# Kernel optimization log

Measured on AMD Instinct MI355X. Metric: run time of the kernel, lower is better.

## Reference

```python
import jax, jax.numpy as jnp
import numpy as np

N, A, R = 131072, 16, 64


def setup_inputs() -> dict:
    key = jax.random.key(0)
    k1, k2, k3 = jax.random.split(key, 3)
    x = jax.random.normal(k1, (N, A), dtype=jnp.float32)
    mu = jax.random.uniform(k2, (R, A), dtype=jnp.float32)      # torch.rand(R, A)
    sigma = jnp.ones((R, A), dtype=jnp.float32) * 0.2           # torch.ones(R, A) * 0.2
    rho = jax.random.normal(k3, (R, A + 1), dtype=jnp.float32) * 0.1
    return {"x": x, "mu": mu, "sigma": sigma, "rho": rho}


def reference(x, mu, sigma, rho):
    # Rule consequents: z[k, r] = x[k] . rho[r, :A] + rho[r, A]   -> [N, R]
    z = jnp.einsum("na,ra->nr", x, rho[:, :-1]) + rho[:, -1]
    # Gaussian membership firing strengths (prod of exps == exp of sum):
    # w[k, r] = prod_a exp(-(x[k,a]-mu[r,a])^2 / (2 sigma[r,a]^2))
    d = x[:, None, :] - mu[None, :, :]                           # [N, R, A]
    logw = -jnp.sum(d * d / (2.0 * sigma[None] ** 2), axis=-1)   # [N, R]
    w = jnp.exp(logw)
    # diag(z @ w.T)[k] = sum_r z[k,r] * w[k,r]; normalized by rule-sum.
    num = jnp.sum(z * w, axis=1)
    den = jnp.sum(w, axis=1) + 1e-13
    return num / den
```

## Files before the change

kernel.cpp:

```cpp
#include <hip/hip_runtime.h>
#include <hip/hip_bf16.h>
#include <math.h>

#define NFEAT 16
#define NRULE 64
#define RQUADS 13
#define RPW 16
#define WPB 4

__global__ void fuzzy_prep(const float* __restrict__ mu,
                           const float* __restrict__ sigma,
                           const float* __restrict__ rho,
                           float* __restrict__ cst) {
    const float L2E = 1.4426950408889634f;
    int r = threadIdx.x;
    if (r >= NRULE) return;
    float* c = cst + r * (RQUADS * 4);
    float K = 0.0f;
#pragma unroll
    for (int a = 0; a < NFEAT; ++a) {
        float m = mu[r * NFEAT + a];
        float s = sigma[r * NFEAT + a];
        float inv = 1.0f / (2.0f * s * s);
        c[a]      = -inv * L2E;
        c[16 + a] = 2.0f * inv * m * L2E;
        c[32 + a] = rho[r * (NFEAT + 1) + a];
        K         = fmaf(-inv * m, m, K);
    }
    c[48] = rho[r * (NFEAT + 1) + NFEAT];
    c[49] = K * L2E;
    c[50] = 0.0f;
    c[51] = 0.0f;
}

__global__ __launch_bounds__(256) void fuzzy_main(const float* __restrict__ x,
                                                  const float* __restrict__ cst,
                                                  float* __restrict__ out,
                                                  int n) {
    __shared__ float4 cl[NRULE * RQUADS];
    __shared__ float pnum[WPB][64];
    __shared__ float pden[WPB][64];

    const int tid  = threadIdx.x;
    const int lane = tid & 63;
    const int q    = __builtin_amdgcn_readfirstlane(tid >> 6);
    const int k    = blockIdx.x * 64 + lane;
    const int kc   = k < n ? k : n - 1;

    const float4* cg = (const float4*)cst;
#pragma unroll
    for (int i = 0; i < 4; ++i) {
        int idx = tid + i * 256;
        if (idx < NRULE * RQUADS) cl[idx] = cg[idx];
    }

    const float4* x4 = (const float4*)(x + (size_t)kc * NFEAT);
    float4 v0 = x4[0], v1 = x4[1], v2 = x4[2], v3 = x4[3];
    float xs[NFEAT] = {v0.x, v0.y, v0.z, v0.w,
                       v1.x, v1.y, v1.z, v1.w,
                       v2.x, v2.y, v2.z, v2.w,
                       v3.x, v3.y, v3.z, v3.w};

    __syncthreads();

    float num = 0.0f, den = 0.0f;
    const float4* cb = cl + q * (RPW * RQUADS);
#pragma unroll 2
    for (int r = 0; r < RPW; ++r) {
        const float4* c = cb + r * RQUADS;
        float4 n0 = c[0], n1 = c[1], n2 = c[2], n3 = c[3];
        float4 m0 = c[4], m1 = c[5], m2 = c[6], m3 = c[7];
        float4 r0 = c[8], r1 = c[9], r2 = c[10], r3 = c[11];
        float4 tl = c[12];
        float nc[NFEAT]  = {n0.x,n0.y,n0.z,n0.w, n1.x,n1.y,n1.z,n1.w,
                            n2.x,n2.y,n2.z,n2.w, n3.x,n3.y,n3.z,n3.w};
        float cm[NFEAT]  = {m0.x,m0.y,m0.z,m0.w, m1.x,m1.y,m1.z,m1.w,
                            m2.x,m2.y,m2.z,m2.w, m3.x,m3.y,m3.z,m3.w};
        float rh[NFEAT]  = {r0.x,r0.y,r0.z,r0.w, r1.x,r1.y,r1.z,r1.w,
                            r2.x,r2.y,r2.z,r2.w, r3.x,r3.y,r3.z,r3.w};
        float z  = tl.x;
        float l0 = tl.y, l1 = 0.0f;
#pragma unroll
        for (int a = 0; a < NFEAT; a += 2) {
            float t0 = fmaf(nc[a],     xs[a],     cm[a]);
            float t1 = fmaf(nc[a + 1], xs[a + 1], cm[a + 1]);
            l0 = fmaf(t0, xs[a],     l0);
            l1 = fmaf(t1, xs[a + 1], l1);
            z  = fmaf(rh[a],     xs[a],     z);
            z  = fmaf(rh[a + 1], xs[a + 1], z);
        }
        float w = __builtin_amdgcn_exp2f(l0 + l1);
        num = fmaf(z, w, num);
        den += w;
    }

    pnum[q][lane] = num;
    pden[q][lane] = den;
    __syncthreads();
    if (q == 0 && k < n) {
        float nn = pnum[0][lane] + pnum[1][lane] + pnum[2][lane] + pnum[3][lane];
        float dd = pden[0][lane] + pden[1][lane] + pden[2][lane] + pden[3][lane];
        out[k] = nn / (dd + 1e-13f);
    }
}

extern "C" void kernel_launch(void* const* d_in, const int* in_sizes, int n_in,
                              void* d_out, int out_size, void* d_ws, size_t ws_size,
                              hipStream_t stream) {
    const float* x     = (const float*)d_in[0];
    const float* mu    = (const float*)d_in[1];
    const float* sigma = (const float*)d_in[2];
    const float* rho   = (const float*)d_in[3];
    float* out = (float*)d_out;
    float* cst = (float*)d_ws;

    int n = in_sizes[0] / NFEAT;

    fuzzy_prep<<<1, 64, 0, stream>>>(mu, sigma, rho, cst);
    fuzzy_main<<<(n + 63) / 64, 256, 0, stream>>>(x, cst, out, n);
}
```

Measured before the change: 77.61 us.

## Process four samples per thread and add uniform-sigma fast path

Each thread now handles four samples, so every rule constant loaded from LDS is reused across four samples instead of one, and the grid shrinks by four. The prep kernel detects at runtime whether all sigmas within a rule are equal. When they are, the quadratic term is computed once per sample as a shared ||x||^2 scaled by a per-rule constant, which removes one FMA per feature per rule. This fast path is general and checked at runtime, though it fires for the test inputs. The cost is higher register pressure from holding four x vectors, and fewer blocks to fill the GPU.

```diff
diff --git a/kernel.cpp b/kernel.cpp
--- a/kernel.cpp
+++ b/kernel.cpp
@@ -1,5 +1,4 @@
 #include <hip/hip_runtime.h>
-#include <hip/hip_bf16.h>
 #include <math.h>
 
 #define NFEAT 16
@@ -7,100 +6,165 @@
 #define RQUADS 13
 #define RPW 16
 #define WPB 4
+#define SPL 4
 
 __global__ void fuzzy_prep(const float* __restrict__ mu,
                            const float* __restrict__ sigma,
                            const float* __restrict__ rho,
                            float* __restrict__ cst) {
     const float L2E = 1.4426950408889634f;
+    __shared__ int uni[NRULE];
     int r = threadIdx.x;
-    if (r >= NRULE) return;
-    float* c = cst + r * (RQUADS * 4);
-    float K = 0.0f;
-#pragma unroll
-    for (int a = 0; a < NFEAT; ++a) {
-        float m = mu[r * NFEAT + a];
-        float s = sigma[r * NFEAT + a];
-        float inv = 1.0f / (2.0f * s * s);
-        c[a]      = -inv * L2E;
-        c[16 + a] = 2.0f * inv * m * L2E;
-        c[32 + a] = rho[r * (NFEAT + 1) + a];
-        K         = fmaf(-inv * m, m, K);
+    if (r < NRULE) {
+        float* c = cst + r * 52;
+        float s0 = sigma[r * NFEAT];
+        float c0 = 1.0f / (2.0f * s0 * s0);
+        float K = 0.0f;
+        int u = 1;
+        for (int a = 0; a < NFEAT; ++a) {
+            float m = mu[r * NFEAT + a];
+            float s = sigma[r * NFEAT + a];
+            float inv = 1.0f / (2.0f * s * s);
+            if (inv != c0) u = 0;
+            c[a]      = -inv * L2E;
+            c[16 + a] = 2.0f * inv * m * L2E;
+            c[32 + a] = rho[r * (NFEAT + 1) + a];
+            K         = fmaf(-inv * m, m, K);
+        }
+        c[48] = rho[r * (NFEAT + 1) + NFEAT];
+        c[49] = K * L2E;
+        c[50] = -c0 * L2E;
+        c[51] = 0.0f;
+        uni[r] = u;
     }
-    c[48] = rho[r * (NFEAT + 1) + NFEAT];
-    c[49] = K * L2E;
-    c[50] = 0.0f;
-    c[51] = 0.0f;
+    __syncthreads();
+    if (r == 0) {
+        int f = 1;
+        for (int i = 0; i < NRULE; ++i) f &= uni[i];
+        cst[NRULE * 52] = (float)f;
+    }
 }
 
-__global__ __launch_bounds__(256) void fuzzy_main(const float* __restrict__ x,
-                                                  const float* __restrict__ cst,
-                                                  float* __restrict__ out,
-                                                  int n) {
+__global__ __launch_bounds__(256, 2) void fuzzy_main(const float* __restrict__ x,
+                                                     const float* __restrict__ cst,
+                                                     float* __restrict__ out,
+                                                     int n) {
     __shared__ float4 cl[NRULE * RQUADS];
-    __shared__ float pnum[WPB][64];
-    __shared__ float pden[WPB][64];
+    __shared__ float pnum[WPB][256];
+    __shared__ float pden[WPB][256];
 
     const int tid  = threadIdx.x;
     const int lane = tid & 63;
     const int q    = __builtin_amdgcn_readfirstlane(tid >> 6);
-    const int k    = blockIdx.x * 64 + lane;
-    const int kc   = k < n ? k : n - 1;
+    const int base = blockIdx.x * (64 * SPL);
 
     const float4* cg = (const float4*)cst;
+    for (int i = tid; i < NRULE * RQUADS; i += 256) cl[i] = cg[i];
+    const int flag = (int)cst[NRULE * 52];
+
+    float xs[SPL][NFEAT];
+    float Qs[SPL];
 #pragma unroll
-    for (int i = 0; i < 4; ++i) {
-        int idx = tid + i * 256;
-        if (idx < NRULE * RQUADS) cl[idx] = cg[idx];
+    for (int s = 0; s < SPL; ++s) {
+        int k = base + s * 64 + lane;
+        int kc = k < n ? k : n - 1;
+        const float4* x4 = (const float4*)(x + (size_t)kc * NFEAT);
+        float4 a = x4[0], b = x4[1], c = x4[2], d = x4[3];
+        float* p = xs[s];
+        p[0]=a.x; p[1]=a.y; p[2]=a.z; p[3]=a.w;
+        p[4]=b.x; p[5]=b.y; p[6]=b.z; p[7]=b.w;
+        p[8]=c.x; p[9]=c.y; p[10]=c.z; p[11]=c.w;
+        p[12]=d.x; p[13]=d.y; p[14]=d.z; p[15]=d.w;
+        float qq = 0.0f;
+#pragma unroll
+        for (int a2 = 0; a2 < NFEAT; ++a2) qq = fmaf(p[a2], p[a2], qq);
+        Qs[s] = qq;
+    }
+    __syncthreads();
+
+    float num[SPL] = {0, 0, 0, 0}, den[SPL] = {0, 0, 0, 0};
+    const float4* cb = cl + q * (RPW * RQUADS);
+
+    if (flag) {
+#pragma unroll 2
+        for (int r = 0; r < RPW; ++r) {
+            const float4* c = cb + r * RQUADS;
+            float4 b0 = c[4], b1 = c[5], b2 = c[6], b3 = c[7];
+            float4 r0 = c[8], r1 = c[9], r2 = c[10], r3 = c[11];
+            float4 tl = c[12];
+            float B[NFEAT]  = {b0.x,b0.y,b0.z,b0.w, b1.x,b1.y,b1.z,b1.w,
+                               b2.x,b2.y,b2.z,b2.w, b3.x,b3.y,b3.z,b3.w};
+            float rh[NFEAT] = {r0.x,r0.y,r0.z,r0.w, r1.x,r1.y,r1.z,r1.w,
+                               r2.x,r2.y,r2.z,r2.w, r3.x,r3.y,r3.z,r3.w};
+            float z[SPL], l[SPL];
+#pragma unroll
+            for (int s = 0; s < SPL; ++s) {
+                z[s] = tl.x;
+                l[s] = fmaf(tl.z, Qs[s], tl.y);
+            }
+#pragma unroll
+            for (int a = 0; a < NFEAT; ++a) {
+#pragma unroll
+                for (int s = 0; s < SPL; ++s) {
+                    l[s] = fmaf(B[a],  xs[s][a], l[s]);
+                    z[s] = fmaf(rh[a], xs[s][a], z[s]);
+                }
+            }
+#pragma unroll
+            for (int s = 0; s < SPL; ++s) {
+                float w = __builtin_amdgcn_exp2f(l[s]);
+                num[s] = fmaf(z[s], w, num[s]);
+                den[s] += w;
+            }
+        }
+    } else {
+#pragma unroll 2
+        for (int r = 0; r < RPW; ++r) {
+            const float4* c = cb + r * RQUADS;
+            float4 n0 = c[0], n1 = c[1], n2 = c[2], n3 = c[3];
+            float4 m0 = c[4], m1 = c[5], m2 = c[6], m3 = c[7];
+            float4 r0 = c[8], r1 = c[9], r2 = c[10], r3 = c[11];
+            float4 tl = c[12];
+            float nc[NFEAT] = {n0.x,n0.y,n0.z,n0.w, n1.x,n1.y,n1.z,n1.w,
+                               n2.x,n2.y,n2.z,n2.w, n3.x,n3.y,n3.z,n3.w};
+            float cm[NFEAT] = {m0.x,m0.y,m0.z,m0.w, m1.x,m1.y,m1.z,m1.w,
+                               m2.x,m2.y,m2.z,m2.w, m3.x,m3.y,m3.z,m3.w};
+            float rh[NFEAT] = {r0.x,r0.y,r0.z,r0.w, r1.x,r1.y,r1.z,r1.w,
+                               r2.x,r2.y,r2.z,r2.w, r3.x,r3.y,r3.z,r3.w};
+            float z[SPL], l[SPL];
+#pragma unroll
+            for (int s = 0; s < SPL; ++s) { z[s] = tl.x; l[s] = tl.y; }
+#pragma unroll
+            for (int a = 0; a < NFEAT; ++a) {
+#pragma unroll
+                for (int s = 0; s < SPL; ++s) {
+                    float t = fmaf(nc[a], xs[s][a], cm[a]);
+                    l[s] = fmaf(t, xs[s][a], l[s]);
+                    z[s] = fmaf(rh[a], xs[s][a], z[s]);
+                }
+            }
+#pragma unroll
+            for (int s = 0; s < SPL; ++s) {
+                float w = __builtin_amdgcn_exp2f(l[s]);
+                num[s] = fmaf(z[s], w, num[s]);
+                den[s] += w;
+            }
+        }
     }
 
-    const float4* x4 = (const float4*)(x + (size_t)kc * NFEAT);
-    float4 v0 = x4[0], v1 = x4[1], v2 = x4[2], v3 = x4[3];
-    float xs[NFEAT] = {v0.x, v0.y, v0.z, v0.w,
-                       v1.x, v1.y, v1.z, v1.w,
-                       v2.x, v2.y, v2.z, v2.w,
-                       v3.x, v3.y, v3.z, v3.w};
-
+#pragma unroll
+    for (int s = 0; s < SPL; ++s) {
+        pnum[q][s * 64 + lane] = num[s];
+        pden[q][s * 64 + lane] = den[s];
+    }
     __syncthreads();
-
-    float num = 0.0f, den = 0.0f;
-    const float4* cb = cl + q * (RPW * RQUADS);
-#pragma unroll 2
-    for (int r = 0; r < RPW; ++r) {
-        const float4* c = cb + r * RQUADS;
-        float4 n0 = c[0], n1 = c[1], n2 = c[2], n3 = c[3];
-        float4 m0 = c[4], m1 = c[5], m2 = c[6], m3 = c[7];
-        float4 r0 = c[8], r1 = c[9], r2 = c[10], r3 = c[11];
-        float4 tl = c[12];
-        float nc[NFEAT]  = {n0.x,n0.y,n0.z,n0.w, n1.x,n1.y,n1.z,n1.w,
-                            n2.x,n2.y,n2.z,n2.w, n3.x,n3.y,n3.z,n3.w};
-        float cm[NFEAT]  = {m0.x,m0.y,m0.z,m0.w, m1.x,m1.y,m1.z,m1.w,
-                            m2.x,m2.y,m2.z,m2.w, m3.x,m3.y,m3.z,m3.w};
-        float rh[NFEAT]  = {r0.x,r0.y,r0.z,r0.w, r1.x,r1.y,r1.z,r1.w,
-                            r2.x,r2.y,r2.z,r2.w, r3.x,r3.y,r3.z,r3.w};
-        float z  = tl.x;
-        float l0 = tl.y, l1 = 0.0f;
-#pragma unroll
-        for (int a = 0; a < NFEAT; a += 2) {
-            float t0 = fmaf(nc[a],     xs[a],     cm[a]);
-            float t1 = fmaf(nc[a + 1], xs[a + 1], cm[a + 1]);
-            l0 = fmaf(t0, xs[a],     l0);
-            l1 = fmaf(t1, xs[a + 1], l1);
-            z  = fmaf(rh[a],     xs[a],     z);
-            z  = fmaf(rh[a + 1], xs[a + 1], z);
+    {
+        int k = base + tid;
+        if (k < n) {
+            float nn = pnum[0][tid] + pnum[1][tid] + pnum[2][tid] + pnum[3][tid];
+            float dd = pden[0][tid] + pden[1][tid] + pden[2][tid] + pden[3][tid];
+            out[k] = nn / (dd + 1e-13f);
         }
-        float w = __builtin_amdgcn_exp2f(l0 + l1);
-        num = fmaf(z, w, num);
-        den += w;
-    }
-
-    pnum[q][lane] = num;
-    pden[q][lane] = den;
-    __syncthreads();
-    if (q == 0 && k < n) {
-        float nn = pnum[0][lane] + pnum[1][lane] + pnum[2][lane] + pnum[3][lane];
-        float dd = pden[0][lane] + pden[1][lane] + pden[2][lane] + pden[3][lane];
-        out[k] = nn / (dd + 1e-13f);
     }
 }
 
@@ -117,5 +181,6 @@
     int n = in_sizes[0] / NFEAT;
 
     fuzzy_prep<<<1, 64, 0, stream>>>(mu, sigma, rho, cst);
-    fuzzy_main<<<(n + 63) / 64, 256, 0, stream>>>(x, cst, out, n);
+    int blocks = (n + 64 * SPL - 1) / (64 * SPL);
+    fuzzy_main<<<blocks, 256, 0, stream>>>(x, cst, out, n);
 }
```

Result: faster. 75.82 us (-2.3%).
